# Optimization experiments

Hardware: AMD Instinct MI355X
Metric: run time of the kernel (lower is better)

Reference implementation:

```python
import jax, jax.numpy as jnp
import numpy as np

B, T_ENC, C, H, NSTEPS, NCLS, NEMB = 512, 64, 512, 512, 26, 97, 256


def setup_inputs() -> dict:
    key = jax.random.key(0)
    ks = jax.random.split(key, 20)
    w = lambda k, shape, s=0.05: jax.random.normal(k, shape, dtype=jnp.float32) * s
    return {
        "batch_H": jax.random.normal(ks[0], (B, T_ENC, C), dtype=jnp.float32),
        "Attentive_Sequence": jax.random.normal(ks[1], (B, NSTEPS, H), dtype=jnp.float32),
        "text": jax.random.randint(ks[2], (B, NSTEPS), 0, NCLS),
        "W_i2h": w(ks[3], (H, C)),                      # i2h, bias=False
        "W_h2h": w(ks[4], (H, H)), "b_h2h": w(ks[5], (H,)),
        "w_score": w(ks[6], (H,)),                      # score Linear(H,1), bias=False
        "W_ih": w(ks[7], (4 * H, C + NEMB)), "W_hh": w(ks[8], (4 * H, H)),
        "b_ih": w(ks[9], (4 * H,)), "b_hh": w(ks[10], (4 * H,)),
        "Wf1": w(ks[11], (H, H)), "bf1": w(ks[12], (H,)),   # GatedBimodal branch 1
        "Wf2": w(ks[13], (H, H)), "bf2": w(ks[14], (H,)),   # GatedBimodal branch 2
        "Wz": w(ks[15], (H, 2 * H)), "bz": w(ks[16], (H,)),  # gate over concat
        "W_gen": w(ks[17], (NCLS, H)), "b_gen": w(ks[18], (NCLS,)),
        "emb_table": w(ks[19], (NCLS + 1, NEMB), 1.0),
    }


def reference(batch_H, Attentive_Sequence, text, W_i2h, W_h2h, b_h2h, w_score,
              W_ih, W_hh, b_ih, b_hh, Wf1, bf1, Wf2, bf2, Wz, bz,
              W_gen, b_gen, emb_table):
    b = batch_H.shape[0]
    char_embs = emb_table[text]                                  # [B, NSTEPS, NEMB]
    H_proj = jnp.einsum('btc,hc->bth', batch_H, W_i2h)           # i2h once (loop-invariant)
    h0 = jnp.zeros((b, H), jnp.float32)
    c0 = jnp.zeros((b, H), jnp.float32)

    def step(carry, xs):
        h, c = carry
        emb_t, seq_t = xs                                        # [B,NEMB], [B,H]
        hp = h @ W_h2h.T + b_h2h                                 # h2h
        e = jnp.tanh(H_proj + hp[:, None, :]) @ w_score          # [B, T_ENC]
        alpha = jax.nn.softmax(e, axis=1)
        context = jnp.einsum('bt,btc->bc', alpha, batch_H)       # bmm(alpha^T, H)
        # GatedBimodal fusion
        f1 = jnp.tanh(context @ Wf1.T + bf1)
        f2 = jnp.tanh(seq_t @ Wf2.T + bf2)
        z = jax.nn.sigmoid(jnp.concatenate([context, seq_t], axis=1) @ Wz.T + bz)
        I_char = z * f1 + (1.0 - z) * f2
        # LSTMCell
        x = jnp.concatenate([I_char, emb_t], axis=1)
        gates = x @ W_ih.T + b_ih + h @ W_hh.T + b_hh
        i_g, f_g, g_g, o_g = jnp.split(gates, 4, axis=1)
        c_new = jax.nn.sigmoid(f_g) * c + jax.nn.sigmoid(i_g) * jnp.tanh(g_g)
        h_new = jax.nn.sigmoid(o_g) * jnp.tanh(c_new)
        return (h_new, c_new), (h_new, alpha, I_char)

    xs = (jnp.swapaxes(char_embs, 0, 1), jnp.swapaxes(Attentive_Sequence, 0, 1))
    _, (hs, alphas, chars) = jax.lax.scan(step, (h0, c0), xs)
    output_hiddens = jnp.swapaxes(hs, 0, 1)                      # [B, NSTEPS, H]
    seq_attention_map = jnp.transpose(alphas, (1, 2, 0))         # [B, T_ENC, NSTEPS]
    Char = jnp.swapaxes(chars, 0, 1)                             # [B, NSTEPS, H]
    probs = output_hiddens @ W_gen.T + b_gen                     # [B, NSTEPS, NCLS]
    return probs, seq_attention_map, output_hiddens, Char
```

## Files before the change

### kernel.cpp

```cpp
#include <hip/hip_runtime.h>

#define NS_ 26
#define NCLS_ 97

typedef short bf16x8 __attribute__((ext_vector_type(8)));
typedef float f32x4 __attribute__((ext_vector_type(4)));

__device__ __forceinline__ unsigned short f2bf(float f) {
  union { float f; unsigned u; } v; v.f = f;
  unsigned r = v.u + 0x7fffu + ((v.u >> 16) & 1u);
  return (unsigned short)(r >> 16);
}
__device__ __forceinline__ float bf2f(unsigned short h) {
  union { unsigned u; float f; } v; v.u = ((unsigned)h) << 16;
  return v.f;
}
__device__ __forceinline__ float sigm_f(float x) { return 1.f / (1.f + __expf(-x)); }
__device__ __forceinline__ float tanh_f(float x) { return 1.f - 2.f / (1.f + __expf(2.f * x)); }

__device__ __forceinline__ void gl_lds16(const void* g, void* l) {
  __builtin_amdgcn_global_load_lds(
      (const __attribute__((address_space(1))) unsigned int*)g,
      (__attribute__((address_space(3))) unsigned int*)l, 16, 0, 0);
}

__device__ __forceinline__ bf16x8 llcld(const unsigned short* p) {
  bf16x8 v;
  asm volatile("global_load_dwordx4 %0, %1, off sc0 sc1\ns_waitcnt vmcnt(0)"
               : "=v"(v) : "v"(p) : "memory");
  return v;
}
__device__ __forceinline__ void llcst(unsigned short* p, bf16x8 v) {
  asm volatile("global_store_dwordx4 %0, %1, off sc0 sc1" :: "v"(p), "v"(v) : "memory");
}
__device__ __forceinline__ f32x4 llcldf(const float* p) {
  f32x4 v;
  asm volatile("global_load_dwordx4 %0, %1, off sc0 sc1\ns_waitcnt vmcnt(0)"
               : "=v"(v) : "v"(p) : "memory");
  return v;
}
__device__ __forceinline__ void llcstf(float* p, f32x4 v) {
  asm volatile("global_store_dwordx4 %0, %1, off sc0 sc1" :: "v"(p), "v"(v) : "memory");
}

__device__ __forceinline__ void gbar(unsigned* bar, unsigned* gen, unsigned target) {
  asm volatile("s_waitcnt vmcnt(0)" ::: "memory");
  __syncthreads();
  if (threadIdx.x == 0) {
    const unsigned prev = __hip_atomic_fetch_add(bar, 1u, __ATOMIC_RELAXED, __HIP_MEMORY_SCOPE_AGENT);
    if (prev + 1u == target * 32u) {
      __hip_atomic_store(gen, target, __ATOMIC_RELAXED, __HIP_MEMORY_SCOPE_AGENT);
    } else {
      while (__hip_atomic_load(gen, __ATOMIC_RELAXED, __HIP_MEMORY_SCOPE_AGENT) < target) {}
    }
  }
  __syncthreads();
}

template <bool OUTF>
__global__ __launch_bounds__(256) void gemm_tiled_k(
    const unsigned short* __restrict__ Ag, const unsigned short* __restrict__ Bg,
    const float* __restrict__ bias, float* __restrict__ outF,
    unsigned short* __restrict__ outB, int K, long ldo, int Nvalid) {
  __shared__ unsigned short As[128 * 64];
  __shared__ unsigned short Bs[128 * 64];
  const int tid = threadIdx.x;
  const int w = tid >> 6, l = tid & 63;
  const int l15 = l & 15, lq = l >> 4;
  const int wm = w >> 1, wn = w & 1;
  const long rowBase = (long)blockIdx.y * 128;
  const long colBase = (long)blockIdx.x * 128;
  const int lrow = l >> 3, ps_st = l & 7;
  f32x4 acc[4][4] = {};
  for (int kt = 0; kt < K; kt += 64) {
#pragma unroll
    for (int i = 0; i < 4; ++i) {
      const int row = i * 32 + w * 8 + lrow;
      const int ls = ps_st ^ (row & 7);
      gl_lds16(Ag + (rowBase + row) * K + kt + ls * 8, As + i * 2048 + w * 512);
      gl_lds16(Bg + (colBase + row) * K + kt + ls * 8, Bs + i * 2048 + w * 512);
    }
    __syncthreads();
#pragma unroll
    for (int kh = 0; kh < 2; ++kh) {
      bf16x8 af[4], bfr[4];
#pragma unroll
      for (int mi = 0; mi < 4; ++mi) {
        const int row = wm * 64 + mi * 16 + l15;
        const int ps = (kh * 4 + lq) ^ (row & 7);
        af[mi] = *(const bf16x8*)(As + row * 64 + ps * 8);
      }
#pragma unroll
      for (int ni = 0; ni < 4; ++ni) {
        const int row = wn * 64 + ni * 16 + l15;
        const int ps = (kh * 4 + lq) ^ (row & 7);
        bfr[ni] = *(const bf16x8*)(Bs + row * 64 + ps * 8);
      }
#pragma unroll
      for (int mi = 0; mi < 4; ++mi)
#pragma unroll
        for (int ni = 0; ni < 4; ++ni)
          acc[mi][ni] = __builtin_amdgcn_mfma_f32_16x16x32_bf16(af[mi], bfr[ni], acc[mi][ni], 0, 0, 0);
    }
    __syncthreads();
  }
#pragma unroll
  for (int mi = 0; mi < 4; ++mi)
#pragma unroll
    for (int ni = 0; ni < 4; ++ni) {
      const long gcol = colBase + wn * 64 + ni * 16 + l15;
      if (gcol >= Nvalid) continue;
      const float bv = bias ? bias[gcol] : 0.f;
#pragma unroll
      for (int r = 0; r < 4; ++r) {
        const long grow = rowBase + wm * 64 + mi * 16 + lq * 4 + r;
        const float v = acc[mi][ni][r] + bv;
        if (OUTF) outF[grow * ldo + gcol] = v;
        else      outB[grow * ldo + gcol] = f2bf(v);
      }
    }
}

struct CoopArgs {
  const unsigned short* Hproj;
  const unsigned short* bH;
  const unsigned short* Wh2hb;
  const unsigned short* Wfz;
  const unsigned short* FZpre;
  const unsigned short* Wihh;
  const unsigned short* embb;
  const float* b_h2h;
  const float* w_score;
  const float* bf1;
  const float* biasG;
  float* hp;
  float* out_attn;
  float* out_char;
  float* out_hid;
  float* cbuf;
  unsigned short* ctx;
  unsigned short* Ichar;
  unsigned short* hbuf;
  unsigned* bars;
};

__global__ __launch_bounds__(1024, 4) void scan_coop_k(CoopArgs A) {
  __shared__ float ws_t[520];
  __shared__ __align__(16) char smraw[52224];
  const int tid = threadIdx.x;
  const int bx = blockIdx.x;
  const int g = bx & 7, lb = bx >> 3;
  const long rb = (long)g * 64;
  unsigned* bar = A.bars + g * 32;
  unsigned* gen = bar + 1;
  unsigned tgt = 0;

  if (tid < 512) ws_t[(tid & 7) * 65 + (tid >> 3)] = A.w_score[tid];
  __syncthreads();

  for (int s = 0; s < NS_; ++s) {
    const unsigned short* hrd = A.hbuf + (s & 1) * 262144;
    unsigned short* hwr = A.hbuf + ((s + 1) & 1) * 262144;

    {
      const int bt = lb >> 3, jt = lb & 7;
      const long b0 = rb + bt * 16;
      const int j0 = jt * 64;
      unsigned short* h16 = (unsigned short*)smraw;
      float* ls = (float*)(smraw + 16640);
      float* hpo = (float*)(smraw + 24960);
      {
        const int row = tid >> 6, c = tid & 63;
        const bf16x8 v = llcld(hrd + (b0 + row) * 512 + c * 8);
        *(bf16x8*)(h16 + row * 520 + c * 8) = v;
      }
      __syncthreads();
      if (tid < 512) {
        const int w = tid >> 6, l = tid & 63, l15 = l & 15, lq = l >> 4;
        const int kh = w >> 2, ni = w & 3;
        const unsigned short* wrow = A.Wh2hb + (long)(j0 + ni * 16 + l15) * 512 + kh * 256;
        const unsigned short* arow = h16 + l15 * 520 + kh * 256;
        f32x4 acc = {};
#pragma unroll
        for (int kt = 0; kt < 256; kt += 64) {
          const int k0 = kt + lq * 8, k1 = k0 + 32;
          const bf16x8 a0 = *(const bf16x8*)(arow + k0);
          const bf16x8 a1 = *(const bf16x8*)(arow + k1);
          const bf16x8 w0 = *(const bf16x8*)(wrow + k0);
          const bf16x8 w1 = *(const bf16x8*)(wrow + k1);
          acc = __builtin_amdgcn_mfma_f32_16x16x32_bf16(a0, w0, acc, 0, 0, 0);
          acc = __builtin_amdgcn_mfma_f32_16x16x32_bf16(a1, w1, acc, 0, 0, 0);
        }
#pragma unroll
        for (int r = 0; r < 4; ++r)
          ls[kh * 1040 + (lq * 4 + r) * 65 + ni * 16 + l15] = acc[r];
      }
      __syncthreads();
      {
        const int r = tid >> 6, c = tid & 63;
        hpo[r * 64 + c] = ls[r * 65 + c] + ls[1040 + r * 65 + c] + A.b_h2h[j0 + c];
      }
      __syncthreads();
      if (tid < 256) {
        const int row = tid >> 4, c = tid & 15;
        const f32x4 v = *(const f32x4*)(hpo + row * 64 + c * 4);
        llcstf(A.hp + (b0 + row) * 512 + j0 + c * 4, v);
      }
    }
    gbar(bar, gen, ++tgt);

    {
      const long b0 = rb + lb * 2;
      float* hp_t = (float*)smraw;
      float* e_s  = (float*)(smraw + 4160);
      float* part = (float*)(smraw + 4672);
      float* colsum = (float*)(smraw + 37952);
      if (tid < 256) {
        const int row = tid >> 7, q = tid & 127;
        const f32x4 v = llcldf(A.hp + (b0 + row) * 512 + q * 4);
#pragma unroll
        for (int i = 0; i < 4; ++i) {
          const int j = q * 4 + i;
          hp_t[row * 520 + (j & 7) * 65 + (j >> 3)] = v[i];
        }
      }
      __syncthreads();
      const int w16 = tid >> 6, l = tid & 63;
      const int srow = w16 >> 3;
      const float* hpT = hp_t + srow * 520;
#pragma unroll
      for (int tt = 0; tt < 8; ++tt) {
        const int t = (w16 & 7) * 8 + tt;
        const bf16x8 hv = *(const bf16x8*)(A.Hproj + ((b0 + srow) * 64 + t) * 512 + l * 8);
        float acc = 0.f;
#pragma unroll
        for (int j = 0; j < 8; ++j)
          acc += tanh_f(bf2f((unsigned short)hv[j]) + hpT[j * 65 + l]) * ws_t[j * 65 + l];
        acc += __shfl_xor(acc, 1);
        acc += __shfl_xor(acc, 2);
        acc += __shfl_xor(acc, 4);
        acc += __shfl_xor(acc, 8);
        acc += __shfl_xor(acc, 16);
        acc += __shfl_xor(acc, 32);
        if (l == 0) e_s[srow * 64 + t] = acc;
      }
      __syncthreads();
      if ((w16 & 7) == 0) {
        const float e = e_s[srow * 64 + l];
        float m = e;
        for (int off = 32; off; off >>= 1) m = fmaxf(m, __shfl_xor(m, off));
        const float p = __expf(e - m);
        float sum = p;
        for (int off = 32; off; off >>= 1) sum += __shfl_xor(sum, off);
        const float a = p / sum;
        e_s[srow * 64 + l] = a;
        A.out_attn[((b0 + srow) * 64 + l) * NS_ + s] = a;
      }
      __syncthreads();
      {
        const int ssb = tid >> 9;
        const int sstid = tid & 511;
        const long b = b0 + ssb;
        const int tg = sstid >> 6;
        const int c8 = sstid & 63;
        const float* al = e_s + ssb * 64 + tg * 8;
        const unsigned short* bhp = A.bH + (b * 64 + tg * 8) * 512 + c8 * 8;
        float a8[8] = {};
#pragma unroll
        for (int tt = 0; tt < 8; ++tt) {
          const bf16x8 v = *(const bf16x8*)(bhp + (long)tt * 512);
          const float a = al[tt];
#pragma unroll
          for (int j = 0; j < 8; ++j) a8[j] += a * bf2f((unsigned short)v[j]);
        }
        float* pp = part + ssb * 4160 + tg * 520 + c8 * 8;
#pragma unroll
        for (int j = 0; j < 8; ++j) pp[j] = a8[j];
      }
      __syncthreads();
      {
        const int ssb = tid >> 9;
        const int j = tid & 511;
        const float* pp = part + ssb * 4160 + j;
        const float sum = pp[0] + pp[520] + pp[1040] + pp[1560]
                        + pp[2080] + pp[2600] + pp[3120] + pp[3640];
        colsum[ssb * 512 + j] = sum;
      }
      __syncthreads();
      {
        const int ssb = tid >> 9;
        const int sstid = tid & 511;
        if (sstid < 64) {
          const float* cs = colsum + ssb * 512 + sstid * 8;
          bf16x8 v;
#pragma unroll
          for (int j = 0; j < 8; ++j) v[j] = (short)f2bf(cs[j]);
          llcst(A.ctx + (b0 + ssb) * 512 + sstid * 8, v);
        }
      }
    }
    gbar(bar, gen, ++tgt);

    {
      const int j0 = (lb & 7) * 64;
      const long b0 = rb + (lb >> 3) * 16;
      unsigned short* ctxs = (unsigned short*)smraw;
      float* ls = (float*)(smraw + 16640);
      unsigned short* ist = (unsigned short*)(smraw + 24960);
      {
        const int row = tid >> 6, c = tid & 63;
        const bf16x8 v = llcld(A.ctx + (b0 + row) * 512 + c * 8);
        *(bf16x8*)(ctxs + row * 520 + c * 8) = v;
      }
      __syncthreads();
      if (tid < 512) {
        const int w = tid >> 6, l = tid & 63, l15 = l & 15, lq = l >> 4;
        const int which = w >> 2, nh = w & 3;
        f32x4 acc = {};
        const long gw = (long)(which ? 512 : 0) + j0 + nh * 16 + l15;
#pragma unroll
        for (int kt = 0; kt < 512; kt += 64) {
          const int k0 = kt + lq * 8, k1 = k0 + 32;
          const bf16x8 a0 = *(const bf16x8*)(ctxs + l15 * 520 + k0);
          const bf16x8 a1 = *(const bf16x8*)(ctxs + l15 * 520 + k1);
          const bf16x8 w0 = *(const bf16x8*)(A.Wfz + gw * 512 + k0);
          const bf16x8 w1 = *(const bf16x8*)(A.Wfz + gw * 512 + k1);
          acc = __builtin_amdgcn_mfma_f32_16x16x32_bf16(a0, w0, acc, 0, 0, 0);
          acc = __builtin_amdgcn_mfma_f32_16x16x32_bf16(a1, w1, acc, 0, 0, 0);
        }
#pragma unroll
        for (int r = 0; r < 4; ++r)
          ls[which * 1040 + (lq * 4 + r) * 65 + nh * 16 + l15] = acc[r];
      }
      __syncthreads();
      {
        const int r = tid >> 6, c = tid & 63;
        const long b = b0 + r;
        const int j = j0 + c;
        const float f1 = tanh_f(ls[r * 65 + c] + A.bf1[j]);
        const float zc = ls[1040 + r * 65 + c];
        const long pr = (b * NS_ + s) * 1024;
        const float f2 = tanh_f(bf2f(A.FZpre[pr + j]));
        const float z = sigm_f(zc + bf2f(A.FZpre[pr + 512 + j]));
        const float I = z * f1 + (1.f - z) * f2;
        A.out_char[(b * NS_ + s) * 512 + j] = I;
        ist[r * 64 + c] = f2bf(I);
      }
      __syncthreads();
      if (tid < 128) {
        const int row = tid >> 3, c = tid & 7;
        const bf16x8 v = *(const bf16x8*)(ist + row * 64 + c * 8);
        llcst(A.Ichar + (b0 + row) * 512 + j0 + c * 8, v);
      }
    }
    gbar(bar, gen, ++tgt);

    {
      const int bt = lb & 3, jp = lb >> 2;
      const long b0 = rb + bt * 16;
      unsigned short* ichs = (unsigned short*)smraw;
      unsigned short* hss = (unsigned short*)(smraw + 16640);
      float* gs = (float*)(smraw + 33280);
      unsigned short* hst = (unsigned short*)(smraw + 50176);
      for (int t = tid; t < 2048; t += 1024) {
        const int arr = t >> 10, q = t & 1023;
        const int row = q >> 6, c = q & 63;
        if (arr == 0) {
          const bf16x8 v = llcld(A.Ichar + (b0 + row) * 512 + c * 8);
          *(bf16x8*)(ichs + row * 520 + c * 8) = v;
        } else {
          const bf16x8 v = llcld(hrd + (b0 + row) * 512 + c * 8);
          *(bf16x8*)(hss + row * 520 + c * 8) = v;
        }
      }
      __syncthreads();
      {
        const int sb = tid >> 9, st = tid & 511;
        const int w = st >> 6, l = st & 63, l15 = l & 15, lq = l >> 4;
        const int g4 = w & 3, ni = w >> 2;
        const int j0 = jp * 64 + sb * 32;
        const unsigned short* wptr = A.Wihh + ((long)g4 * 512 + j0 + ni * 16 + l15) * 1280;
        const unsigned short* eptr = A.embb + ((b0 + l15) * NS_ + s) * 256;
        f32x4 acc = {};
#pragma unroll
        for (int kt = 0; kt < 1280; kt += 64) {
          const int k0 = kt + lq * 8, k1 = k0 + 32;
          bf16x8 a0, a1;
          a0 = (k0 < 512) ? *(const bf16x8*)(ichs + l15 * 520 + k0)
             : (k0 < 768) ? *(const bf16x8*)(eptr + (k0 - 512))
                          : *(const bf16x8*)(hss + l15 * 520 + (k0 - 768));
          a1 = (k1 < 512) ? *(const bf16x8*)(ichs + l15 * 520 + k1)
             : (k1 < 768) ? *(const bf16x8*)(eptr + (k1 - 512))
                          : *(const bf16x8*)(hss + l15 * 520 + (k1 - 768));
          const bf16x8 w0 = *(const bf16x8*)(wptr + k0);
          const bf16x8 w1 = *(const bf16x8*)(wptr + k1);
          acc = __builtin_amdgcn_mfma_f32_16x16x32_bf16(a0, w0, acc, 0, 0, 0);
          acc = __builtin_amdgcn_mfma_f32_16x16x32_bf16(a1, w1, acc, 0, 0, 0);
        }
        float* gss = gs + sb * 2112;
#pragma unroll
        for (int r = 0; r < 4; ++r)
          gss[(g4 * 16 + lq * 4 + r) * 33 + ni * 16 + l15] = acc[r];
      }
      __syncthreads();
      {
        const int sb = tid >> 9, e = tid & 511;
        const int r = e >> 5, c = e & 31;
        const long b = b0 + r;
        const int j = jp * 64 + sb * 32 + c;
        const float* gss = gs + sb * 2112;
        const float ig = sigm_f(gss[(0 * 16 + r) * 33 + c] + A.biasG[j]);
        const float fg = sigm_f(gss[(1 * 16 + r) * 33 + c] + A.biasG[512 + j]);
        const float gg = tanh_f(gss[(2 * 16 + r) * 33 + c] + A.biasG[1024 + j]);
        const float og = sigm_f(gss[(3 * 16 + r) * 33 + c] + A.biasG[1536 + j]);
        const float cn = fg * A.cbuf[b * 512 + j] + ig * gg;
        A.cbuf[b * 512 + j] = cn;
        const float h = og * tanh_f(cn);
        A.out_hid[(b * NS_ + s) * 512 + j] = h;
        hst[sb * 512 + r * 32 + c] = f2bf(h);
      }
      __syncthreads();
      if (tid < 128) {
        const int sb = tid >> 6, q = tid & 63;
        const int row = q >> 2, c = q & 3;
        const bf16x8 v = *(const bf16x8*)(hst + sb * 512 + row * 32 + c * 8);
        llcst(hwr + (b0 + row) * 512 + jp * 64 + sb * 32 + c * 8, v);
      }
    }
    gbar(bar, gen, ++tgt);
  }
}

__global__ __launch_bounds__(256) void probs_k(
    const float* __restrict__ Af, const unsigned short* __restrict__ Wg,
    const float* __restrict__ bias, float* __restrict__ outp) {
  const int tid = threadIdx.x, w = tid >> 6, l = tid & 63, l15 = l & 15, lq = l >> 4;
  const long mrow = (long)blockIdx.y * 64 + w * 16 + l15;
  const int nbase = blockIdx.x * 64;
  f32x4 acc[4] = {};
  for (int kt = 0; kt < 512; kt += 32) {
    const int k = kt + lq * 8;
    const float4 av0 = *(const float4*)(Af + mrow * 512 + k);
    const float4 av1 = *(const float4*)(Af + mrow * 512 + k + 4);
    bf16x8 a;
    a[0] = (short)f2bf(av0.x); a[1] = (short)f2bf(av0.y);
    a[2] = (short)f2bf(av0.z); a[3] = (short)f2bf(av0.w);
    a[4] = (short)f2bf(av1.x); a[5] = (short)f2bf(av1.y);
    a[6] = (short)f2bf(av1.z); a[7] = (short)f2bf(av1.w);
#pragma unroll
    for (int nb = 0; nb < 4; ++nb) {
      const bf16x8 b = *(const bf16x8*)(Wg + (long)(nbase + nb * 16 + l15) * 512 + k);
      acc[nb] = __builtin_amdgcn_mfma_f32_16x16x32_bf16(a, b, acc[nb], 0, 0, 0);
    }
  }
#pragma unroll
  for (int nb = 0; nb < 4; ++nb) {
    const int colg = nbase + nb * 16 + l15;
    if (colg >= NCLS_) continue;
    const float bv = bias[colg];
#pragma unroll
    for (int r = 0; r < 4; ++r) {
      const long rowg = (long)blockIdx.y * 64 + w * 16 + lq * 4 + r;
      outp[rowg * NCLS_ + colg] = acc[nb][r] + bv;
    }
  }
}

#define CVT_N0 4194304L
#define CVT_N1 1703936L
#define CVT_N2 65536L
__global__ void mega_cvt_k(const float* __restrict__ batch_H, const float* __restrict__ AS,
                           const float* __restrict__ W_i2h,
                           unsigned short* __restrict__ bH, unsigned short* __restrict__ ASb,
                           unsigned short* __restrict__ Wi2hb) {
  const long q = (long)blockIdx.x * 256 + threadIdx.x;
  const float* src; unsigned short* dst; long i;
  if (q < CVT_N0) { src = batch_H; dst = bH; i = q; }
  else if (q < CVT_N0 + CVT_N1) { src = AS; dst = ASb; i = q - CVT_N0; }
  else if (q < CVT_N0 + CVT_N1 + CVT_N2) { src = W_i2h; dst = Wi2hb; i = q - CVT_N0 - CVT_N1; }
  else return;
  const float4 v = *(const float4*)(src + i * 4);
  ushort4 o;
  o.x = f2bf(v.x); o.y = f2bf(v.y); o.z = f2bf(v.z); o.w = f2bf(v.w);
  *(ushort4*)(dst + i * 4) = o;
}

#define PK_N0 2621440L
#define PK_N1 524288L
#define PK_N2 524288L
#define PK_N3 65536L
#define PK_N4 262144L
#define PK_N5 3072L
#define PK_N6 3407872L
__global__ void mega_pack_k(
    const float* __restrict__ W_ih, const float* __restrict__ W_hh,
    const float* __restrict__ Wf1, const float* __restrict__ Wf2,
    const float* __restrict__ Wz, const float* __restrict__ W_gen,
    const float* __restrict__ W_h2h,
    const float* __restrict__ b_ih, const float* __restrict__ b_hh,
    const float* __restrict__ bf2, const float* __restrict__ bz,
    const float* __restrict__ emb_table, const int* __restrict__ text,
    unsigned short* __restrict__ Wihh, unsigned short* __restrict__ Wfz,
    unsigned short* __restrict__ Wfz2, unsigned short* __restrict__ Wgenb,
    unsigned short* __restrict__ Wh2hb, float* __restrict__ biasG,
    float* __restrict__ biasFZ, unsigned short* __restrict__ embb) {
  long q = (long)blockIdx.x * 256 + threadIdx.x;
  if (q < PK_N0) {
    const int row = (int)(q / 1280), c = (int)(q % 1280);
    const float v = (c < 768) ? W_ih[(long)row * 768 + c] : W_hh[(long)row * 512 + (c - 768)];
    Wihh[q] = f2bf(v);
    return;
  }
  q -= PK_N0;
  if (q < PK_N1) {
    const int row = (int)(q >> 9), k = (int)(q & 511);
    const float v = (row < 512) ? Wf1[(long)row * 512 + k] : Wz[(long)(row - 512) * 1024 + k];
    Wfz[q] = f2bf(v);
    return;
  }
  q -= PK_N1;
  if (q < PK_N2) {
    const int row = (int)(q >> 9), k = (int)(q & 511);
    const float v = (row < 512) ? Wf2[(long)row * 512 + k]
                                : Wz[(long)(row - 512) * 1024 + 512 + k];
    Wfz2[q] = f2bf(v);
    return;
  }
  q -= PK_N2;
  if (q < PK_N3) {
    const int row = (int)(q >> 9), k = (int)(q & 511);
    Wgenb[q] = (row < NCLS_) ? f2bf(W_gen[(long)row * 512 + k]) : (unsigned short)0;
    return;
  }
  q -= PK_N3;
  if (q < PK_N4) {
    Wh2hb[q] = f2bf(W_h2h[q]);
    return;
  }
  q -= PK_N4;
  if (q < PK_N5) {
    if (q < 2048) biasG[q] = b_ih[q] + b_hh[q];
    else {
      const int j = (int)(q - 2048);
      biasFZ[j] = (j < 512) ? bf2[j] : bz[j - 512];
    }
    return;
  }
  q -= PK_N5;
  if (q < PK_N6) {
    const long bs = q >> 8;
    const int j = (int)(q & 255);
    const int t = text[bs];
    embb[q] = f2bf(emb_table[(long)t * 256 + j]);
  }
}

extern "C" void kernel_launch(void* const* d_in, const int* in_sizes, int n_in,
                              void* d_out, int out_size, void* d_ws, size_t ws_size,
                              hipStream_t stream) {
  (void)in_sizes; (void)n_in; (void)out_size; (void)ws_size;
  const float* batch_H  = (const float*)d_in[0];
  const float* AS       = (const float*)d_in[1];
  const int*   text     = (const int*)d_in[2];
  const float* W_i2h    = (const float*)d_in[3];
  const float* W_h2h    = (const float*)d_in[4];
  const float* b_h2h    = (const float*)d_in[5];
  const float* w_score  = (const float*)d_in[6];
  const float* W_ih     = (const float*)d_in[7];
  const float* W_hh     = (const float*)d_in[8];
  const float* b_ih     = (const float*)d_in[9];
  const float* b_hh     = (const float*)d_in[10];
  const float* Wf1      = (const float*)d_in[11];
  const float* bf1      = (const float*)d_in[12];
  const float* Wf2      = (const float*)d_in[13];
  const float* bf2      = (const float*)d_in[14];
  const float* Wz       = (const float*)d_in[15];
  const float* bz       = (const float*)d_in[16];
  const float* W_gen    = (const float*)d_in[17];
  const float* b_gen    = (const float*)d_in[18];
  const float* emb_tab  = (const float*)d_in[19];

  float* out = (float*)d_out;
  float* out_probs = out;
  float* out_attn  = out + 1291264;
  float* out_hid   = out + 2143232;
  float* out_char  = out + 8958976;

  char* wsp = (char*)d_ws;
  auto alloc = [&](size_t bytes) { char* p = wsp; wsp += (bytes + 255) & ~(size_t)255; return p; };
  unsigned short* bH    = (unsigned short*)alloc(33554432);
  unsigned short* Hproj = (unsigned short*)alloc(33554432);
  unsigned short* ASb   = (unsigned short*)alloc(13631488);
  unsigned short* embb  = (unsigned short*)alloc(6815744);
  unsigned short* FZpre = (unsigned short*)alloc(27262976);
  unsigned short* Wh2hb = (unsigned short*)alloc(524288);
  unsigned short* Wfz   = (unsigned short*)alloc(1048576);
  unsigned short* Wfz2  = (unsigned short*)alloc(1048576);
  unsigned short* Wihh  = (unsigned short*)alloc(5242880);
  unsigned short* Wgenb = (unsigned short*)alloc(131072);
  unsigned short* Wi2hb = (unsigned short*)alloc(524288);
  float* biasG          = (float*)alloc(8192);
  float* biasFZ         = (float*)alloc(4096);
  unsigned* bars        = (unsigned*)alloc(1024);
  char* ab = (char*)ASb;
  unsigned short* ctx   = (unsigned short*)(ab);
  unsigned short* Ichar = (unsigned short*)(ab + 524288);
  float* cbuf           = (float*)(ab + 1048576);
  unsigned short* hbuf  = (unsigned short*)(ab + 2097152);
  float* hp             = (float*)(ab + 3145728);

  mega_cvt_k<<<dim3(23297), dim3(256), 0, stream>>>(batch_H, AS, W_i2h, bH, ASb, Wi2hb);
  mega_pack_k<<<dim3(28960), dim3(256), 0, stream>>>(
      W_ih, W_hh, Wf1, Wf2, Wz, W_gen, W_h2h, b_ih, b_hh, bf2, bz, emb_tab, text,
      Wihh, Wfz, Wfz2, Wgenb, Wh2hb, biasG, biasFZ, embb);

  gemm_tiled_k<false><<<dim3(4, 256), dim3(256), 0, stream>>>(
      bH, Wi2hb, nullptr, nullptr, Hproj, 512, 512, 512);

  gemm_tiled_k<false><<<dim3(8, 104), dim3(256), 0, stream>>>(
      ASb, Wfz2, biasFZ, nullptr, FZpre, 512, 1024, 1024);

  hipMemsetAsync(cbuf, 0, 1048576, stream);
  hipMemsetAsync(hbuf, 0, 1048576, stream);
  hipMemsetAsync(bars, 0, 1024, stream);

  CoopArgs ca;
  ca.Hproj = Hproj; ca.bH = bH; ca.Wh2hb = Wh2hb; ca.Wfz = Wfz; ca.FZpre = FZpre;
  ca.Wihh = Wihh; ca.embb = embb;
  ca.b_h2h = b_h2h; ca.w_score = w_score; ca.bf1 = bf1; ca.biasG = biasG;
  ca.hp = hp; ca.out_attn = out_attn; ca.out_char = out_char; ca.out_hid = out_hid;
  ca.cbuf = cbuf; ca.ctx = ctx; ca.Ichar = Ichar; ca.hbuf = hbuf; ca.bars = bars;
  void* kargs[] = { (void*)&ca };
  hipLaunchCooperativeKernel((const void*)scan_coop_k, dim3(256), dim3(1024), kargs, 0, stream);

  probs_k<<<dim3(2, 208), dim3(256), 0, stream>>>(out_hid, Wgenb, b_gen, out_probs);
}
```

Before: 1.645 ms.

## Compute h2h projection per block redundantly to drop a grid barrier per step

The h2h projection was previously split across the group's blocks as MFMA tiles, written to a global hp buffer, and followed by a grid barrier. Now each block computes the full 512-wide h2h output for its own two batch rows with scalar FMAs over a transposed, 4-interleaved bf16 weight layout, so hp stays in shared memory. This removes one grid-wide barrier and a global round trip per step. In exchange every block reads the whole W_h2h each step, and the matvec runs on vector ALUs instead of matrix cores.

```diff
diff --git a/kernel.cpp b/kernel.cpp
--- a/kernel.cpp
+++ b/kernel.cpp
@@ -31,15 +31,6 @@
   return v;
 }
 __device__ __forceinline__ void llcst(unsigned short* p, bf16x8 v) {
-  asm volatile("global_store_dwordx4 %0, %1, off sc0 sc1" :: "v"(p), "v"(v) : "memory");
-}
-__device__ __forceinline__ f32x4 llcldf(const float* p) {
-  f32x4 v;
-  asm volatile("global_load_dwordx4 %0, %1, off sc0 sc1\ns_waitcnt vmcnt(0)"
-               : "=v"(v) : "v"(p) : "memory");
-  return v;
-}
-__device__ __forceinline__ void llcstf(float* p, f32x4 v) {
   asm volatile("global_store_dwordx4 %0, %1, off sc0 sc1" :: "v"(p), "v"(v) : "memory");
 }
 
@@ -124,7 +115,7 @@
 struct CoopArgs {
   const unsigned short* Hproj;
   const unsigned short* bH;
-  const unsigned short* Wh2hb;
+  const unsigned short* Wt4;
   const unsigned short* Wfz;
   const unsigned short* FZpre;
   const unsigned short* Wihh;
@@ -133,7 +124,6 @@
   const float* w_score;
   const float* bf1;
   const float* biasG;
-  float* hp;
   float* out_attn;
   float* out_char;
   float* out_hid;
@@ -163,66 +153,42 @@
     unsigned short* hwr = A.hbuf + ((s + 1) & 1) * 262144;
 
     {
-      const int bt = lb >> 3, jt = lb & 7;
-      const long b0 = rb + bt * 16;
-      const int j0 = jt * 64;
-      unsigned short* h16 = (unsigned short*)smraw;
-      float* ls = (float*)(smraw + 16640);
-      float* hpo = (float*)(smraw + 24960);
-      {
+      const long b0 = rb + lb * 2;
+      float* hs     = (float*)smraw;
+      float* gpart  = (float*)(smraw + 4096);
+      float* hp_t   = (float*)(smraw + 12288);
+      float* e_s    = (float*)(smraw + 16448);
+      float* cpart  = (float*)(smraw + 16960);
+      float* colsum = (float*)(smraw + 4096);
+      if (tid < 128) {
         const int row = tid >> 6, c = tid & 63;
         const bf16x8 v = llcld(hrd + (b0 + row) * 512 + c * 8);
-        *(bf16x8*)(h16 + row * 520 + c * 8) = v;
-      }
-      __syncthreads();
-      if (tid < 512) {
-        const int w = tid >> 6, l = tid & 63, l15 = l & 15, lq = l >> 4;
-        const int kh = w >> 2, ni = w & 3;
-        const unsigned short* wrow = A.Wh2hb + (long)(j0 + ni * 16 + l15) * 512 + kh * 256;
-        const unsigned short* arow = h16 + l15 * 520 + kh * 256;
-        f32x4 acc = {};
-#pragma unroll
-        for (int kt = 0; kt < 256; kt += 64) {
-          const int k0 = kt + lq * 8, k1 = k0 + 32;
-          const bf16x8 a0 = *(const bf16x8*)(arow + k0);
-          const bf16x8 a1 = *(const bf16x8*)(arow + k1);
-          const bf16x8 w0 = *(const bf16x8*)(wrow + k0);
-          const bf16x8 w1 = *(const bf16x8*)(wrow + k1);
-          acc = __builtin_amdgcn_mfma_f32_16x16x32_bf16(a0, w0, acc, 0, 0, 0);
-          acc = __builtin_amdgcn_mfma_f32_16x16x32_bf16(a1, w1, acc, 0, 0, 0);
+#pragma unroll
+        for (int j = 0; j < 8; ++j) hs[row * 512 + c * 8 + j] = bf2f((unsigned short)v[j]);
+      }
+      __syncthreads();
+      {
+        const int half = tid >> 9, j = tid & 511;
+        const unsigned short* wp = A.Wt4 + (long)half * 64 * 2048 + j * 4;
+        const float* h0 = hs;
+        const float* h1 = hs + 512;
+        float a0 = 0.f, a1 = 0.f;
+#pragma unroll 8
+        for (int k4 = 0; k4 < 64; ++k4) {
+          const ushort4 wv = *(const ushort4*)(wp + k4 * 2048);
+          const int kb = (half * 64 + k4) * 4;
+          const float w0 = bf2f(wv.x), w1 = bf2f(wv.y), w2 = bf2f(wv.z), w3 = bf2f(wv.w);
+          a0 += w0 * h0[kb] + w1 * h0[kb + 1] + w2 * h0[kb + 2] + w3 * h0[kb + 3];
+          a1 += w0 * h1[kb] + w1 * h1[kb + 1] + w2 * h1[kb + 2] + w3 * h1[kb + 3];
         }
-#pragma unroll
-        for (int r = 0; r < 4; ++r)
-          ls[kh * 1040 + (lq * 4 + r) * 65 + ni * 16 + l15] = acc[r];
-      }
-      __syncthreads();
-      {
-        const int r = tid >> 6, c = tid & 63;
-        hpo[r * 64 + c] = ls[r * 65 + c] + ls[1040 + r * 65 + c] + A.b_h2h[j0 + c];
-      }
-      __syncthreads();
-      if (tid < 256) {
-        const int row = tid >> 4, c = tid & 15;
-        const f32x4 v = *(const f32x4*)(hpo + row * 64 + c * 4);
-        llcstf(A.hp + (b0 + row) * 512 + j0 + c * 4, v);
-      }
-    }
-    gbar(bar, gen, ++tgt);
-
-    {
-      const long b0 = rb + lb * 2;
-      float* hp_t = (float*)smraw;
-      float* e_s  = (float*)(smraw + 4160);
-      float* part = (float*)(smraw + 4672);
-      float* colsum = (float*)(smraw + 37952);
-      if (tid < 256) {
-        const int row = tid >> 7, q = tid & 127;
-        const f32x4 v = llcldf(A.hp + (b0 + row) * 512 + q * 4);
-#pragma unroll
-        for (int i = 0; i < 4; ++i) {
-          const int j = q * 4 + i;
-          hp_t[row * 520 + (j & 7) * 65 + (j >> 3)] = v[i];
-        }
+        gpart[half * 1024 + j] = a0;
+        gpart[half * 1024 + 512 + j] = a1;
+      }
+      __syncthreads();
+      {
+        const int pair = tid >> 9, j = tid & 511;
+        const float hpv = gpart[pair * 512 + j] + gpart[1024 + pair * 512 + j] + A.b_h2h[j];
+        hp_t[pair * 520 + (j & 7) * 65 + (j >> 3)] = hpv;
       }
       __syncthreads();
       const int w16 = tid >> 6, l = tid & 63;
@@ -273,7 +239,7 @@
 #pragma unroll
           for (int j = 0; j < 8; ++j) a8[j] += a * bf2f((unsigned short)v[j]);
         }
-        float* pp = part + ssb * 4160 + tg * 520 + c8 * 8;
+        float* pp = cpart + ssb * 4160 + tg * 520 + c8 * 8;
 #pragma unroll
         for (int j = 0; j < 8; ++j) pp[j] = a8[j];
       }
@@ -281,7 +247,7 @@
       {
         const int ssb = tid >> 9;
         const int j = tid & 511;
-        const float* pp = part + ssb * 4160 + j;
+        const float* pp = cpart + ssb * 4160 + j;
         const float sum = pp[0] + pp[520] + pp[1040] + pp[1560]
                         + pp[2080] + pp[2600] + pp[3120] + pp[3640];
         colsum[ssb * 512 + j] = sum;
@@ -502,7 +468,7 @@
     const float* __restrict__ emb_table, const int* __restrict__ text,
     unsigned short* __restrict__ Wihh, unsigned short* __restrict__ Wfz,
     unsigned short* __restrict__ Wfz2, unsigned short* __restrict__ Wgenb,
-    unsigned short* __restrict__ Wh2hb, float* __restrict__ biasG,
+    unsigned short* __restrict__ Wt4, float* __restrict__ biasG,
     float* __restrict__ biasFZ, unsigned short* __restrict__ embb) {
   long q = (long)blockIdx.x * 256 + threadIdx.x;
   if (q < PK_N0) {
@@ -534,7 +500,8 @@
   }
   q -= PK_N3;
   if (q < PK_N4) {
-    Wh2hb[q] = f2bf(W_h2h[q]);
+    const int j = (int)(q >> 9), k = (int)(q & 511);
+    Wt4[((long)(k >> 2) * 2048) + j * 4 + (k & 3)] = f2bf(W_h2h[q]);
     return;
   }
   q -= PK_N4;
@@ -593,7 +560,7 @@
   unsigned short* ASb   = (unsigned short*)alloc(13631488);
   unsigned short* embb  = (unsigned short*)alloc(6815744);
   unsigned short* FZpre = (unsigned short*)alloc(27262976);
-  unsigned short* Wh2hb = (unsigned short*)alloc(524288);
+  unsigned short* Wt4   = (unsigned short*)alloc(524288);
   unsigned short* Wfz   = (unsigned short*)alloc(1048576);
   unsigned short* Wfz2  = (unsigned short*)alloc(1048576);
   unsigned short* Wihh  = (unsigned short*)alloc(5242880);
@@ -607,12 +574,11 @@
   unsigned short* Ichar = (unsigned short*)(ab + 524288);
   float* cbuf           = (float*)(ab + 1048576);
   unsigned short* hbuf  = (unsigned short*)(ab + 2097152);
-  float* hp             = (float*)(ab + 3145728);
 
   mega_cvt_k<<<dim3(23297), dim3(256), 0, stream>>>(batch_H, AS, W_i2h, bH, ASb, Wi2hb);
   mega_pack_k<<<dim3(28960), dim3(256), 0, stream>>>(
       W_ih, W_hh, Wf1, Wf2, Wz, W_gen, W_h2h, b_ih, b_hh, bf2, bz, emb_tab, text,
-      Wihh, Wfz, Wfz2, Wgenb, Wh2hb, biasG, biasFZ, embb);
+      Wihh, Wfz, Wfz2, Wgenb, Wt4, biasG, biasFZ, embb);
 
   gemm_tiled_k<false><<<dim3(4, 256), dim3(256), 0, stream>>>(
       bH, Wi2hb, nullptr, nullptr, Hproj, 512, 512, 512);
@@ -625,10 +591,10 @@
   hipMemsetAsync(bars, 0, 1024, stream);
 
   CoopArgs ca;
-  ca.Hproj = Hproj; ca.bH = bH; ca.Wh2hb = Wh2hb; ca.Wfz = Wfz; ca.FZpre = FZpre;
+  ca.Hproj = Hproj; ca.bH = bH; ca.Wt4 = Wt4; ca.Wfz = Wfz; ca.FZpre = FZpre;
   ca.Wihh = Wihh; ca.embb = embb;
   ca.b_h2h = b_h2h; ca.w_score = w_score; ca.bf1 = bf1; ca.biasG = biasG;
-  ca.hp = hp; ca.out_attn = out_attn; ca.out_char = out_char; ca.out_hid = out_hid;
+  ca.out_attn = out_attn; ca.out_char = out_char; ca.out_hid = out_hid;
   ca.cbuf = cbuf; ca.ctx = ctx; ca.Ichar = Ichar; ca.hbuf = hbuf; ca.bars = bars;
   void* kargs[] = { (void*)&ca };
   hipLaunchCooperativeKernel((const void*)scan_coop_k, dim3(256), dim3(1024), kargs, 0, stream);
```

After: 2.019 ms. 1.23x slower.
